# Optimization experiments

Measured on AMD Instinct MI355X. Metric: run time of the kernel, lower is better.

The kernel has to match this reference:

```python
import jax, jax.numpy as jnp
import numpy as np

K_SIZE = 7
D_MODEL = 128
D_Q = 64
N_HEADS = 4
D_FF = 512
EPS = 1e-5


def _windows(x, k):
    # x: [N,E,H,W] -> [N,E,P,H,W]; zero-padded local k x k windows,
    # row-major over (dy,dx), matching nn.Unfold ordering.
    p = k // 2
    N, E, H, W = x.shape
    xp = jnp.pad(x, ((0, 0), (0, 0), (p, p), (p, p)))
    ws = [xp[:, :, i:i + H, j:j + W] for i in range(k) for j in range(k)]
    return jnp.stack(ws, axis=2)


def _layernorm(x, g, b):
    m = jnp.mean(x, -1, keepdims=True)
    v = jnp.var(x, -1, keepdims=True)
    return (x - m) * jax.lax.rsqrt(v + EPS) * g + b


def setup_inputs() -> dict:
    key = jax.random.key(0)
    ks = jax.random.split(key, 12)
    E, Q, F = D_MODEL, D_Q, D_FF

    def g(k, shape, s=0.02):
        return jax.random.normal(k, shape, jnp.float32) * s

    return dict(
        x=jax.random.normal(ks[0], (4, E, 64, 64), jnp.float32),
        qcoeff=jax.random.normal(ks[1], (4, Q), jnp.float32),
        wq=g(ks[2], (E, E)), bq=jnp.zeros((E,), jnp.float32),
        wk=g(ks[3], (E, E)), bk=jnp.zeros((E,), jnp.float32),
        wv=g(ks[4], (E, E)), bv=jnp.zeros((E,), jnp.float32),
        rel_bias=jnp.zeros((N_HEADS, K_SIZE * K_SIZE), jnp.float32),
        ln1_g=jnp.ones((E,), jnp.float32), ln1_b=jnp.zeros((E,), jnp.float32),
        bil_w=g(ks[5], (E, E, Q)), bil_b=jnp.zeros((E,), jnp.float32),
        ln2_g=jnp.ones((E,), jnp.float32), ln2_b=jnp.zeros((E,), jnp.float32),
        w1=g(ks[6], (F, E)), b1=jnp.zeros((F,), jnp.float32),
        w2=g(ks[7], (E, F)), b2=jnp.zeros((E,), jnp.float32),
    )


def reference(x, qcoeff, wq, bq, wk, bk, wv, bv, rel_bias, ln1_g, ln1_b,
              bil_w, bil_b, ln2_g, ln2_b, w1, b1, w2, b2):
    N, E, H, W = x.shape
    Nh = N_HEADS
    Hd = E // Nh
    P = K_SIZE * K_SIZE

    x_nhwc = jnp.transpose(x, (0, 2, 3, 1))              # [N,H,W,E]
    xn = _layernorm(x_nhwc, ln1_g, ln1_b)
    xnc = jnp.transpose(xn, (0, 3, 1, 2))                # [N,E,H,W]

    # 1x1-conv projections
    q = jnp.einsum('nchw,oc->nohw', xnc, wq) + bq[None, :, None, None]
    k = jnp.einsum('nchw,oc->nohw', xnc, wk) + bk[None, :, None, None]
    v = jnp.einsum('nchw,oc->nohw', xnc, wv) + bv[None, :, None, None]

    # local windows of K/V: [N,Nh,Hd,P,H,W]
    Kw = _windows(k, K_SIZE).reshape(N, Nh, Hd, P, H, W)
    Vw = _windows(v, K_SIZE).reshape(N, Nh, Hd, P, H, W)
    Qh = q.reshape(N, Nh, Hd, H, W)

    scores = jnp.einsum('nhdyx,nhdpyx->nhpyx', Qh, Kw)
    scores = scores + rel_bias[None, :, :, None, None]
    attn = jax.nn.softmax(scores, axis=2)                # softmax over P
    out = jnp.einsum('nhpyx,nhdpyx->nhdyx', attn, Vw).reshape(N, E, H, W)
    z0 = jnp.transpose(out, (0, 2, 3, 1))                # [N,H,W,E]

    # Bilinear(z0, qcoeff): qcoeff constant per (H,W) -> contract once per batch
    t = jnp.einsum('oiq,nq->noi', bil_w, qcoeff)         # [N,E,E]
    z1 = jnp.einsum('nhwi,noi->nhwo', z0, t) + bil_b

    z2 = z1 + x_nhwc
    z3 = _layernorm(z2, ln2_g, ln2_b)
    h1 = jax.nn.gelu(z3 @ w1.T + b1, approximate=False)  # dropout inactive (eval)
    z4 = h1 @ w2.T + b2 + z2
    return jnp.transpose(z4, (0, 3, 1, 2))               # [N,E,H,W]
```

## Files before the change

### kernel.cpp

```cpp
#include <hip/hip_runtime.h>
#include <cmath>

#define EPS 1e-5f
#define SZ 2097152

typedef __attribute__((ext_vector_type(8))) short short8;
typedef __attribute__((ext_vector_type(4))) float floatx4;

__device__ __forceinline__ float dot4(float4 a, float4 b) {
  return fmaf(a.x, b.x, fmaf(a.y, b.y, fmaf(a.z, b.z, a.w * b.w)));
}

__device__ __forceinline__ short f2bf(float f) {
  union { float f; unsigned u; } v; v.f = f;
  unsigned r = v.u + 0x7fff + ((v.u >> 16) & 1);
  return (short)(r >> 16);
}

#define MFMA16(a, b, c) __builtin_amdgcn_mfma_f32_16x16x32_bf16(a, b, c, 0, 0, 0)

__global__ __launch_bounds__(256) void k_prep(const float* __restrict__ w1,
    const float* __restrict__ w2, const float* __restrict__ wq,
    const float* __restrict__ wk, const float* __restrict__ wv,
    const float* __restrict__ bil_w, const float* __restrict__ qcoeff,
    short* __restrict__ w1bf, short* __restrict__ w2bf,
    short* __restrict__ wqbf, short* __restrict__ wkbf, short* __restrict__ wvbf,
    short* __restrict__ tb) {
  __shared__ float qs[256];
  int tid = threadIdx.x;
  qs[tid] = qcoeff[tid];
  __syncthreads();
  int tid0 = blockIdx.x * 256 + tid;
  int stride = gridDim.x * 256;
  for (int i = tid0; i < 16384; i += stride) {
    int flat = i * 4; int f = flat >> 7, c = flat & 127;
    float4 v = *(const float4*)&w1[flat];
    short t4[4] = {f2bf(v.x), f2bf(v.y), f2bf(v.z), f2bf(v.w)};
    *(uint2*)&w1bf[f * 136 + c] = *(uint2*)t4;
  }
  for (int i = tid0; i < 16384; i += stride) {
    int flat = i * 4; int o = flat >> 9, j = flat & 511;
    int ck = j >> 7, jj = j & 127;
    float4 v = *(const float4*)&w2[flat];
    short t4[4] = {f2bf(v.x), f2bf(v.y), f2bf(v.z), f2bf(v.w)};
    *(uint2*)&w2bf[(ck * 128 + o) * 136 + jj] = *(uint2*)t4;
  }
  for (int i = tid0; i < 4096; i += stride) {
    int flat = i * 4; int o = flat >> 7, c = flat & 127;
    float4 a = *(const float4*)&wq[flat];
    float4 b = *(const float4*)&wk[flat];
    float4 cc = *(const float4*)&wv[flat];
    short ta[4] = {f2bf(a.x), f2bf(a.y), f2bf(a.z), f2bf(a.w)};
    short tb4[4] = {f2bf(b.x), f2bf(b.y), f2bf(b.z), f2bf(b.w)};
    short tc[4] = {f2bf(cc.x), f2bf(cc.y), f2bf(cc.z), f2bf(cc.w)};
    *(uint2*)&wqbf[o * 136 + c] = *(uint2*)ta;
    *(uint2*)&wkbf[o * 136 + c] = *(uint2*)tb4;
    *(uint2*)&wvbf[o * 136 + c] = *(uint2*)tc;
  }
  for (int flat = tid0; flat < 16384; flat += stride) {
    const float* wrow = bil_w + (size_t)flat * 64;
    float acc[4] = {0.f, 0.f, 0.f, 0.f};
    for (int qq = 0; qq < 64; qq += 4) {
      float4 w4 = *(const float4*)&wrow[qq];
#pragma unroll
      for (int nn = 0; nn < 4; ++nn) {
        const float* qc = &qs[nn * 64 + qq];
        acc[nn] = fmaf(w4.x, qc[0], fmaf(w4.y, qc[1], fmaf(w4.z, qc[2], fmaf(w4.w, qc[3], acc[nn]))));
      }
    }
    int o = flat >> 7, i = flat & 127;
#pragma unroll
    for (int nn = 0; nn < 4; ++nn) tb[nn * 17408 + o * 136 + i] = f2bf(acc[nn]);
  }
}

__global__ __launch_bounds__(512) void k_qkvln(const float* __restrict__ x,
    const float* __restrict__ g, const float* __restrict__ b,
    const short* __restrict__ wqbf, const short* __restrict__ wkbf,
    const short* __restrict__ wvbf, const float* __restrict__ bq,
    const float* __restrict__ bk, const float* __restrict__ bv,
    float* __restrict__ xnhwc, short* __restrict__ qbf,
    short* __restrict__ kbf, short* __restrict__ vtb) {
  __shared__ float tile[128 * 33];
  __shared__ float mres[32], rres[32];
  __shared__ __align__(16) short xs[32 * 136];
  __shared__ __align__(16) short ws[128 * 136];
  int tid = threadIdx.x;
  int bid = blockIdx.x;
  int half = bid & 1, ny = bid >> 1;
  int n = ny >> 6, y = ny & 63;
  const float* xb = x + (size_t)n * 524288 + y * 64 + half * 32;
  for (int it = 0; it < 8; ++it) {
    int flat = it * 512 + tid;
    int c = flat >> 5, xpl = flat & 31;
    tile[c * 33 + xpl] = xb[(size_t)c * 4096 + xpl];
  }
  __syncthreads();
  {
    int pxl = tid >> 4, cl = tid & 15;
    float s = 0.f, sq = 0.f;
#pragma unroll
    for (int j = 0; j < 8; ++j) {
      float v = tile[(cl * 8 + j) * 33 + pxl];
      s += v; sq += v * v;
    }
    s += __shfl_xor(s, 1);  sq += __shfl_xor(sq, 1);
    s += __shfl_xor(s, 2);  sq += __shfl_xor(sq, 2);
    s += __shfl_xor(s, 4);  sq += __shfl_xor(sq, 4);
    s += __shfl_xor(s, 8);  sq += __shfl_xor(sq, 8);
    if (cl == 0) {
      float m = s * (1.f / 128.f);
      float var = sq * (1.f / 128.f) - m * m;
      mres[pxl] = m;
      rres[pxl] = rsqrtf(var + EPS);
    }
  }
  __syncthreads();
  size_t rowbase = (size_t)ny * 8192 + half * 4096;
  for (int it = 0; it < 8; ++it) {
    int flat = it * 512 + tid;
    int c = flat & 127, pxl = flat >> 7;
    float v = tile[c * 33 + pxl];
    xnhwc[rowbase + flat] = v;
    xs[pxl * 136 + c] = f2bf((v - mres[pxl]) * rres[pxl] * g[c] + b[c]);
  }
  __syncthreads();
  int w = tid >> 6, lane = tid & 63;
  int quad = lane >> 4, r16 = lane & 15;
  int wm = w & 1, wn = w >> 1;
  int stripl = wm * 16;
  short8 a[4];
#pragma unroll
  for (int kk = 0; kk < 4; ++kk)
    a[kk] = *(const short8*)&xs[(stripl + r16) * 136 + kk * 32 + quad * 8];
  const short* wptr[3] = {wqbf, wkbf, wvbf};
  const float* bptr[3] = {bq, bk, bv};
  for (int m = 0; m < 3; ++m) {
    __syncthreads();
    const short* wp = wptr[m];
    for (int i = tid; i < 2176; i += 512)
      *(short8*)&ws[i * 8] = *(const short8*)&wp[i * 8];
    __syncthreads();
    const float* bb = bptr[m];
#pragma unroll
    for (int nt = 0; nt < 2; ++nt) {
      int o0 = wn * 32 + nt * 16;
      floatx4 acc = {0.f, 0.f, 0.f, 0.f};
#pragma unroll
      for (int kk = 0; kk < 4; ++kk) {
        short8 bfr = *(const short8*)&ws[(o0 + r16) * 136 + kk * 32 + quad * 8];
        acc = MFMA16(a[kk], bfr, acc);
      }
      float bv2 = bb[o0 + r16];
      if (m < 2) {
        short* dst = (m == 0) ? qbf : kbf;
#pragma unroll
        for (int r = 0; r < 4; ++r) {
          int pxl = stripl + quad * 4 + r;
          dst[rowbase + pxl * 128 + o0 + r16] = f2bf(acc[r] + bv2);
        }
      } else {
        short t4[4] = {f2bf(acc[0] + bv2), f2bf(acc[1] + bv2),
                       f2bf(acc[2] + bv2), f2bf(acc[3] + bv2)};
        *(uint2*)&vtb[(size_t)(n * 128 + o0 + r16) * 4096 + y * 64 + half * 32 +
                      stripl + quad * 4] = *(uint2*)t4;
      }
    }
  }
}

__global__ __launch_bounds__(512, 4) void k_at(const short* __restrict__ qbf,
    const short* __restrict__ kbf, const short* __restrict__ vtb,
    const float* __restrict__ rel_bias, const short* __restrict__ tb,
    const float* __restrict__ bil_b, const float* __restrict__ xnhwc,
    const float* __restrict__ g2, const float* __restrict__ b2ln,
    const short* __restrict__ w1bf, const float* __restrict__ b1,
    const short* __restrict__ w2bf, const float* __restrict__ b2,
    float* __restrict__ out) {
  __shared__ __align__(16) char smem[70272];
  short* h1s = (short*)smem;
  short* z3s = (short*)(smem + 44672);
  float* z2s = (float*)(smem + 53376);
  int tid = threadIdx.x;
  int bid = blockIdx.x;
  int half = bid & 1, ny = bid >> 1;
  int n = ny >> 6, y = ny & 63;
  int w16 = tid >> 6, lane = tid & 63;
  int quad = lane >> 4, r16 = lane & 15;
  size_t rowbase = (size_t)ny * 8192;
  int wm = w16 & 1, wn = w16 >> 1;
  int stripL = wm * 16;
  const short* tn = tb + (size_t)n * 17408;
  float xres[2][4];
#pragma unroll
  for (int nt = 0; nt < 2; ++nt)
#pragma unroll
    for (int r = 0; r < 4; ++r)
      xres[nt][r] = xnhwc[rowbase + (half * 32 + stripL + quad * 4 + r) * 128 +
                          wn * 32 + nt * 16 + r16];
  short8 tf[2][4];
  {
    int h = w16 >> 1, swl = w16 & 1;
    int sg = half * 2 + swl;
    int strip = sg * 16;
    float* ssfw = (float*)(smem + w16 * 3200);
    short* Abw = (short*)(smem + 25600 + w16 * 2176);
    float* biasw = (float*)(smem + 43008 + w16 * 208);
    const short* qrow = qbf + (size_t)n * 524288 + (size_t)y * 8192 + h * 32;
    const short* kbp = kbf + (size_t)n * 524288 + h * 32;
    short8 qf = *(const short8*)&qrow[(strip + r16) * 128 + quad * 8];
    short8 kf[7][2];
#pragma unroll
    for (int r = 0; r < 7; ++r) {
      int yyc = min(max(y + r - 3, 0), 63);
#pragma unroll
      for (int t = 0; t < 2; ++t) {
        int gxc = min(max((sg + t) * 16 + r16 - 3, 0), 63);
        kf[r][t] = *(const short8*)&kbp[(size_t)(yyc * 64 + gxc) * 128 + quad * 8];
      }
    }
    {
      unsigned* ad = (unsigned*)Abw;
      for (int i = lane; i < 544; i += 64) ad[i] = 0u;
    }
    if (lane < 49) biasw[lane] = rel_bias[h * 49 + lane];
#pragma unroll
    for (int r = 0; r < 7; ++r) {
      bool yok = (unsigned)(y + r - 3) < 64u;
#pragma unroll
      for (int t = 0; t < 2; ++t) {
        int xxc = (sg + t) * 16 + r16;
        bool ok = yok && ((unsigned)(xxc - 3) < 64u);
        floatx4 c = MFMA16(qf, kf[r][t], ((floatx4){0.f, 0.f, 0.f, 0.f}));
#pragma unroll
        for (int rr = 0; rr < 4; ++rr) {
          int lrow = quad * 4 + rr;
          int dx = xxc - (strip + lrow);
          if ((unsigned)dx < 7u) {
            float val = ok ? c[rr] : 0.f;
            ssfw[lrow * 50 + r * 7 + dx] = val + biasw[r * 7 + dx];
          }
        }
      }
    }
    {
      int lrow = lane >> 2, sub = lane & 3;
      int p0 = sub * 12;
      float sv[13];
      float mx = -1e30f;
#pragma unroll
      for (int pi = 0; pi < 13; ++pi) {
        sv[pi] = ssfw[lrow * 50 + p0 + pi];
        mx = fmaxf(mx, sv[pi]);
      }
      mx = fmaxf(mx, __shfl_xor(mx, 1));
      mx = fmaxf(mx, __shfl_xor(mx, 2));
      float sum = 0.f;
#pragma unroll
      for (int pi = 0; pi < 13; ++pi) {
        float e = __expf(sv[pi] - mx);
        if (pi == 12 && sub != 3) e = 0.f;
        sv[pi] = e; sum += e;
      }
      sum += __shfl_xor(sum, 1);
      sum += __shfl_xor(sum, 2);
      float inv = 1.f / sum;
#pragma unroll
      for (int pi = 0; pi < 13; ++pi)
        if (pi < 12 || sub == 3) ssfw[lrow * 50 + p0 + pi] = sv[pi] * inv;
    }
    floatx4 oacc[2] = {(floatx4){0.f, 0.f, 0.f, 0.f}, (floatx4){0.f, 0.f, 0.f, 0.f}};
    int lrow = lane >> 2, sub = lane & 3;
    int pxg = strip + lrow;
    const short* vbp = vtb + (size_t)(n * 128 + h * 32) * 4096;
    short8 vf[2][2][2];
    {
      int yyc0 = min(max(y - 3, 0), 63);
#pragma unroll
      for (int kk = 0; kk < 2; ++kk)
#pragma unroll
        for (int nt = 0; nt < 2; ++nt)
          vf[0][kk][nt] = *(const short8*)&vbp[(size_t)(nt * 16 + r16) * 4096 + yyc0 * 64 + kk * 32 + quad * 8];
    }
#pragma unroll
    for (int r = 0; r < 7; ++r) {
      if (r < 6) {
        int yycn = min(max(y + r - 2, 0), 63);
#pragma unroll
        for (int kk = 0; kk < 2; ++kk)
#pragma unroll
          for (int nt = 0; nt < 2; ++nt)
            vf[(r + 1) & 1][kk][nt] = *(const short8*)&vbp[(size_t)(nt * 16 + r16) * 4096 + yycn * 64 + kk * 32 + quad * 8];
      }
      int c0 = pxg + sub - 3;
      if ((unsigned)c0 < 64u) Abw[lrow * 68 + c0] = f2bf(ssfw[lrow * 50 + r * 7 + sub]);
      int c1 = pxg + sub + 1;
      if (sub < 3 && (unsigned)c1 < 64u)
        Abw[lrow * 68 + c1] = f2bf(ssfw[lrow * 50 + r * 7 + sub + 4]);
      if ((unsigned)(y + r - 3) < 64u) {
#pragma unroll
        for (int kk = 0; kk < 2; ++kk) {
          short8 af = *(const short8*)&Abw[r16 * 68 + kk * 32 + quad * 8];
#pragma unroll
          for (int nt = 0; nt < 2; ++nt)
            oacc[nt] = MFMA16(af, vf[r & 1][kk][nt], oacc[nt]);
        }
      }
    }
#pragma unroll
    for (int nt = 0; nt < 2; ++nt)
#pragma unroll
      for (int kk = 0; kk < 4; ++kk)
        tf[nt][kk] = *(const short8*)&tn[(wn * 32 + nt * 16 + r16) * 136 + kk * 32 + quad * 8];
#pragma unroll
    for (int nt = 0; nt < 2; ++nt)
#pragma unroll
      for (int rr = 0; rr < 4; ++rr) {
        int pxl = swl * 16 + quad * 4 + rr;
        z3s[pxl * 136 + h * 32 + nt * 16 + r16] = f2bf(oacc[nt][rr]);
      }
  }
  __syncthreads();
  {
    short8 a[4];
#pragma unroll
    for (int kk = 0; kk < 4; ++kk)
      a[kk] = *(const short8*)&z3s[(stripL + r16) * 136 + kk * 32 + quad * 8];
#pragma unroll
    for (int nt = 0; nt < 2; ++nt) {
      int o0 = wn * 32 + nt * 16;
      floatx4 acc = {0.f, 0.f, 0.f, 0.f};
#pragma unroll
      for (int kk = 0; kk < 4; ++kk)
        acc = MFMA16(a[kk], tf[nt][kk], acc);
      float bb = bil_b[o0 + r16];
#pragma unroll
      for (int r = 0; r < 4; ++r) {
        int pxl = stripL + quad * 4 + r;
        z2s[pxl * 132 + o0 + r16] = acc[r] + bb + xres[nt][r];
      }
    }
  }
  __syncthreads();
  short8 wA[2][4];
#pragma unroll
  for (int nt = 0; nt < 2; ++nt)
#pragma unroll
    for (int kk = 0; kk < 4; ++kk)
      wA[nt][kk] = *(const short8*)&w1bf[(wn * 32 + nt * 16 + r16) * 136 + kk * 32 + quad * 8];
  {
    int px = tid >> 4, cl = tid & 15;
    float4 v0 = *(const float4*)&z2s[px * 132 + cl * 8];
    float4 v1 = *(const float4*)&z2s[px * 132 + cl * 8 + 4];
    float s = v0.x + v0.y + v0.z + v0.w + v1.x + v1.y + v1.z + v1.w;
    float sq = dot4(v0, v0) + dot4(v1, v1);
    s += __shfl_xor(s, 1);  sq += __shfl_xor(sq, 1);
    s += __shfl_xor(s, 2);  sq += __shfl_xor(sq, 2);
    s += __shfl_xor(s, 4);  sq += __shfl_xor(sq, 4);
    s += __shfl_xor(s, 8);  sq += __shfl_xor(sq, 8);
    float m = s * (1.f / 128.f);
    float var = sq * (1.f / 128.f) - m * m;
    float rr = rsqrtf(var + EPS);
    int c0 = cl * 8;
    short t8[8];
#pragma unroll
    for (int j = 0; j < 8; ++j) {
      float vv = (j < 4) ? (&v0.x)[j] : (&v1.x)[j - 4];
      t8[j] = f2bf((vv - m) * rr * g2[c0 + j] + b2ln[c0 + j]);
    }
    *(uint4*)&z3s[px * 136 + c0] = *(uint4*)t8;
  }
  __syncthreads();
  floatx4 zacc[2];
  zacc[0] = (floatx4){0.f, 0.f, 0.f, 0.f};
  zacc[1] = (floatx4){0.f, 0.f, 0.f, 0.f};
  for (int fc = 0; fc < 512; fc += 128) {
    short8 wB[2][4];
#pragma unroll
    for (int nt = 0; nt < 2; ++nt)
#pragma unroll
      for (int kk = 0; kk < 4; ++kk)
        wB[nt][kk] = *(const short8*)&w2bf[((fc >> 7) * 128 + wn * 32 + nt * 16 + r16) * 136 + kk * 32 + quad * 8];
    float bb1v[2];
    bb1v[0] = b1[fc + wn * 32 + r16];
    bb1v[1] = b1[fc + wn * 32 + 16 + r16];
    short8 a3[4];
#pragma unroll
    for (int kk = 0; kk < 4; ++kk)
      a3[kk] = *(const short8*)&z3s[(stripL + r16) * 136 + kk * 32 + quad * 8];
    floatx4 hacc[2];
#pragma unroll
    for (int nt = 0; nt < 2; ++nt) {
      hacc[nt] = (floatx4){0.f, 0.f, 0.f, 0.f};
#pragma unroll
      for (int kk = 0; kk < 4; ++kk)
        hacc[nt] = MFMA16(a3[kk], wA[nt][kk], hacc[nt]);
    }
    if (fc < 384) {
#pragma unroll
      for (int nt = 0; nt < 2; ++nt)
#pragma unroll
        for (int kk = 0; kk < 4; ++kk)
          wA[nt][kk] = *(const short8*)&w1bf[(fc + 128 + wn * 32 + nt * 16 + r16) * 136 + kk * 32 + quad * 8];
    }
#pragma unroll
    for (int nt = 0; nt < 2; ++nt) {
      int f0 = wn * 32 + nt * 16;
#pragma unroll
      for (int r = 0; r < 4; ++r) {
        float hv = hacc[nt][r] + bb1v[nt];
        float ge = 0.5f * hv * (1.f + erff(hv * 0.70710678118f));
        h1s[(stripL + quad * 4 + r) * 136 + f0 + r16] = f2bf(ge);
      }
    }
    __syncthreads();
    short8 ah[4];
#pragma unroll
    for (int kk = 0; kk < 4; ++kk)
      ah[kk] = *(const short8*)&h1s[(stripL + r16) * 136 + kk * 32 + quad * 8];
#pragma unroll
    for (int nt = 0; nt < 2; ++nt)
#pragma unroll
      for (int kk = 0; kk < 4; ++kk)
        zacc[nt] = MFMA16(ah[kk], wB[nt][kk], zacc[nt]);
    __syncthreads();
  }
#pragma unroll
  for (int nt = 0; nt < 2; ++nt) {
    int o = wn * 32 + nt * 16 + r16;
    float bb = b2[o];
    float res[4];
#pragma unroll
    for (int r = 0; r < 4; ++r)
      res[r] = zacc[nt][r] + bb + z2s[(stripL + quad * 4 + r) * 132 + o];
    *(float4*)&out[(((size_t)(n * 128 + o)) * 64 + y) * 64 + half * 32 + stripL + quad * 4] =
        *(float4*)res;
  }
}

extern "C" void kernel_launch(void* const* d_in, const int* in_sizes, int n_in,
                              void* d_out, int out_size, void* d_ws, size_t ws_size,
                              hipStream_t stream) {
  const float* x        = (const float*)d_in[0];
  const float* qcoeff   = (const float*)d_in[1];
  const float* wq       = (const float*)d_in[2];
  const float* bq       = (const float*)d_in[3];
  const float* wk       = (const float*)d_in[4];
  const float* bk       = (const float*)d_in[5];
  const float* wv       = (const float*)d_in[6];
  const float* bv       = (const float*)d_in[7];
  const float* rel_bias = (const float*)d_in[8];
  const float* ln1_g    = (const float*)d_in[9];
  const float* ln1_b    = (const float*)d_in[10];
  const float* bil_w    = (const float*)d_in[11];
  const float* bil_b    = (const float*)d_in[12];
  const float* ln2_g    = (const float*)d_in[13];
  const float* ln2_b    = (const float*)d_in[14];
  const float* w1       = (const float*)d_in[15];
  const float* b1       = (const float*)d_in[16];
  const float* w2       = (const float*)d_in[17];
  const float* b2       = (const float*)d_in[18];
  float* out = (float*)d_out;

  float* ws = (float*)d_ws;
  float* x_nhwc = ws;
  short* qbf = (short*)(ws + 2 * SZ);
  short* kbf = qbf + SZ;
  short* vtb = kbf + SZ;
  short* bf     = (short*)(ws + 4 * SZ);
  short* tb     = bf;
  short* w1bf   = bf + 4 * 17408;
  short* w2bf   = w1bf + 512 * 136;
  short* wqbf   = w2bf + 4 * 17408;
  short* wkbf   = wqbf + 17408;
  short* wvbf   = wkbf + 17408;

  k_prep<<<256, 256, 0, stream>>>(w1, w2, wq, wk, wv, bil_w, qcoeff,
                                  w1bf, w2bf, wqbf, wkbf, wvbf, tb);
  k_qkvln<<<512, 512, 0, stream>>>(x, ln1_g, ln1_b, wqbf, wkbf, wvbf,
                                   bq, bk, bv, x_nhwc, qbf, kbf, vtb);
  k_at<<<512, 512, 0, stream>>>(qbf, kbf, vtb, rel_bias, tb, bil_b, x_nhwc,
                                ln2_g, ln2_b, w1bf, b1, w2bf, b2, out);
}
```

Measured before the change: 151.0 us.

## Split fused attention/MLP kernel into separate attention and tail kernels with XCD banding

Splits the fused local-attention plus bilinear/LN/MLP kernel into two kernels: k_attn writes the attention output z3 to a global bf16 buffer, and k_tail reads it back for the bilinear, layernorm and FFN stages. Each kernel uses less shared memory and fewer registers, which allows different occupancy targets (launch bounds 3 and 8). It also remaps block indices so that consecutive image rows land on the same XCD, improving L2 reuse of neighbouring K/V rows. The cost is an extra kernel launch and a global round trip for the z3 intermediate.

After: 188.2 us. 1.25x slower.

```diff
diff --git a/kernel.cpp b/kernel.cpp
--- a/kernel.cpp
+++ b/kernel.cpp
@@ -15,6 +15,10 @@
   union { float f; unsigned u; } v; v.f = f;
   unsigned r = v.u + 0x7fff + ((v.u >> 16) & 1);
   return (short)(r >> 16);
+}
+
+__device__ __forceinline__ int xcd_band(int bid) {
+  return (bid & 7) * 64 + (bid >> 3);
 }
 
 #define MFMA16(a, b, c) __builtin_amdgcn_mfma_f32_16x16x32_bf16(a, b, c, 0, 0, 0)
@@ -86,8 +90,8 @@
   __shared__ __align__(16) short xs[32 * 136];
   __shared__ __align__(16) short ws[128 * 136];
   int tid = threadIdx.x;
-  int bid = blockIdx.x;
-  int half = bid & 1, ny = bid >> 1;
+  int l = xcd_band(blockIdx.x);
+  int half = l & 1, ny = l >> 1;
   int n = ny >> 6, y = ny & 63;
   const float* xb = x + (size_t)n * 524288 + y * 64 + half * 32;
   for (int it = 0; it < 8; ++it) {
@@ -169,21 +173,146 @@
   }
 }
 
-__global__ __launch_bounds__(512, 4) void k_at(const short* __restrict__ qbf,
+__global__ __launch_bounds__(512, 3) void k_attn(const short* __restrict__ qbf,
     const short* __restrict__ kbf, const short* __restrict__ vtb,
-    const float* __restrict__ rel_bias, const short* __restrict__ tb,
-    const float* __restrict__ bil_b, const float* __restrict__ xnhwc,
-    const float* __restrict__ g2, const float* __restrict__ b2ln,
-    const short* __restrict__ w1bf, const float* __restrict__ b1,
-    const short* __restrict__ w2bf, const float* __restrict__ b2,
-    float* __restrict__ out) {
-  __shared__ __align__(16) char smem[70272];
-  short* h1s = (short*)smem;
-  short* z3s = (short*)(smem + 44672);
-  float* z2s = (float*)(smem + 53376);
+    const float* __restrict__ rel_bias, short* __restrict__ z3g) {
+  __shared__ __align__(16) char smem[44672];
   int tid = threadIdx.x;
-  int bid = blockIdx.x;
-  int half = bid & 1, ny = bid >> 1;
+  int l = xcd_band(blockIdx.x);
+  int half = l & 1, ny = l >> 1;
+  int n = ny >> 6, y = ny & 63;
+  int w16 = tid >> 6, lane = tid & 63;
+  int quad = lane >> 4, r16 = lane & 15;
+  size_t rowbase = (size_t)ny * 8192;
+  int h = w16 >> 1, swl = w16 & 1;
+  int sg = half * 2 + swl;
+  int strip = sg * 16;
+  float* ssfw = (float*)(smem + w16 * 3200);
+  short* Abw = (short*)(smem + 25600 + w16 * 2176);
+  float* biasw = (float*)(smem + 43008 + w16 * 208);
+  const short* qrow = qbf + (size_t)n * 524288 + (size_t)y * 8192 + h * 32;
+  const short* kbp = kbf + (size_t)n * 524288 + h * 32;
+  short8 qf = *(const short8*)&qrow[(strip + r16) * 128 + quad * 8];
+  short8 kf[7][2];
+#pragma unroll
+  for (int r = 0; r < 7; ++r) {
+    int yyc = min(max(y + r - 3, 0), 63);
+#pragma unroll
+    for (int t = 0; t < 2; ++t) {
+      int gxc = min(max((sg + t) * 16 + r16 - 3, 0), 63);
+      kf[r][t] = *(const short8*)&kbp[(size_t)(yyc * 64 + gxc) * 128 + quad * 8];
+    }
+  }
+  {
+    unsigned* ad = (unsigned*)Abw;
+    for (int i = lane; i < 544; i += 64) ad[i] = 0u;
+  }
+  if (lane < 49) biasw[lane] = rel_bias[h * 49 + lane];
+#pragma unroll
+  for (int r = 0; r < 7; ++r) {
+    bool yok = (unsigned)(y + r - 3) < 64u;
+#pragma unroll
+    for (int t = 0; t < 2; ++t) {
+      int xxc = (sg + t) * 16 + r16;
+      bool ok = yok && ((unsigned)(xxc - 3) < 64u);
+      floatx4 c = MFMA16(qf, kf[r][t], ((floatx4){0.f, 0.f, 0.f, 0.f}));
+#pragma unroll
+      for (int rr = 0; rr < 4; ++rr) {
+        int lrow = quad * 4 + rr;
+        int dx = xxc - (strip + lrow);
+        if ((unsigned)dx < 7u) {
+          float val = ok ? c[rr] : 0.f;
+          ssfw[lrow * 50 + r * 7 + dx] = val + biasw[r * 7 + dx];
+        }
+      }
+    }
+  }
+  {
+    int lrow = lane >> 2, sub = lane & 3;
+    int p0 = sub * 12;
+    float sv[13];
+    float mx = -1e30f;
+#pragma unroll
+    for (int pi = 0; pi < 13; ++pi) {
+      sv[pi] = ssfw[lrow * 50 + p0 + pi];
+      mx = fmaxf(mx, sv[pi]);
+    }
+    mx = fmaxf(mx, __shfl_xor(mx, 1));
+    mx = fmaxf(mx, __shfl_xor(mx, 2));
+    float sum = 0.f;
+#pragma unroll
+    for (int pi = 0; pi < 13; ++pi) {
+      float e = __expf(sv[pi] - mx);
+      if (pi == 12 && sub != 3) e = 0.f;
+      sv[pi] = e; sum += e;
+    }
+    sum += __shfl_xor(sum, 1);
+    sum += __shfl_xor(sum, 2);
+    float inv = 1.f / sum;
+#pragma unroll
+    for (int pi = 0; pi < 13; ++pi)
+      if (pi < 12 || sub == 3) ssfw[lrow * 50 + p0 + pi] = sv[pi] * inv;
+  }
+  floatx4 oacc[2] = {(floatx4){0.f, 0.f, 0.f, 0.f}, (floatx4){0.f, 0.f, 0.f, 0.f}};
+  int lrow = lane >> 2, sub = lane & 3;
+  int pxg = strip + lrow;
+  const short* vbp = vtb + (size_t)(n * 128 + h * 32) * 4096;
+  short8 vf[2][2][2];
+  {
+    int yyc0 = min(max(y - 3, 0), 63);
+#pragma unroll
+    for (int kk = 0; kk < 2; ++kk)
+#pragma unroll
+      for (int nt = 0; nt < 2; ++nt)
+        vf[0][kk][nt] = *(const short8*)&vbp[(size_t)(nt * 16 + r16) * 4096 + yyc0 * 64 + kk * 32 + quad * 8];
+  }
+#pragma unroll
+  for (int r = 0; r < 7; ++r) {
+    if (r < 6) {
+      int yycn = min(max(y + r - 2, 0), 63);
+#pragma unroll
+      for (int kk = 0; kk < 2; ++kk)
+#pragma unroll
+        for (int nt = 0; nt < 2; ++nt)
+          vf[(r + 1) & 1][kk][nt] = *(const short8*)&vbp[(size_t)(nt * 16 + r16) * 4096 + yycn * 64 + kk * 32 + quad * 8];
+    }
+    int c0 = pxg + sub - 3;
+    if ((unsigned)c0 < 64u) Abw[lrow * 68 + c0] = f2bf(ssfw[lrow * 50 + r * 7 + sub]);
+    int c1 = pxg + sub + 1;
+    if (sub < 3 && (unsigned)c1 < 64u)
+      Abw[lrow * 68 + c1] = f2bf(ssfw[lrow * 50 + r * 7 + sub + 4]);
+    if ((unsigned)(y + r - 3) < 64u) {
+#pragma unroll
+      for (int kk = 0; kk < 2; ++kk) {
+        short8 af = *(const short8*)&Abw[r16 * 68 + kk * 32 + quad * 8];
+#pragma unroll
+        for (int nt = 0; nt < 2; ++nt)
+          oacc[nt] = MFMA16(af, vf[r & 1][kk][nt], oacc[nt]);
+      }
+    }
+  }
+#pragma unroll
+  for (int nt = 0; nt < 2; ++nt)
+#pragma unroll
+    for (int rr = 0; rr < 4; ++rr) {
+      int px = half * 32 + swl * 16 + quad * 4 + rr;
+      z3g[rowbase + px * 128 + h * 32 + nt * 16 + r16] = f2bf(oacc[nt][rr]);
+    }
+}
+
+__global__ __launch_bounds__(512, 8) void k_tail(const short* __restrict__ z3g,
+    const short* __restrict__ tb, const float* __restrict__ bil_b,
+    const float* __restrict__ xnhwc, const float* __restrict__ g2,
+    const float* __restrict__ b2ln, const short* __restrict__ w1bf,
+    const float* __restrict__ b1, const short* __restrict__ w2bf,
+    const float* __restrict__ b2, float* __restrict__ out) {
+  __shared__ __align__(16) char smem[34304];
+  short* z3s = (short*)smem;
+  float* z2s = (float*)(smem + 8704);
+  short* h1s = (short*)(smem + 25600);
+  int tid = threadIdx.x;
+  int l = xcd_band(blockIdx.x);
+  int half = l & 1, ny = l >> 1;
   int n = ny >> 6, y = ny & 63;
   int w16 = tid >> 6, lane = tid & 63;
   int quad = lane >> 4, r16 = lane & 15;
@@ -191,6 +320,12 @@
   int wm = w16 & 1, wn = w16 >> 1;
   int stripL = wm * 16;
   const short* tn = tb + (size_t)n * 17408;
+  short8 tf[2][4];
+#pragma unroll
+  for (int nt = 0; nt < 2; ++nt)
+#pragma unroll
+    for (int kk = 0; kk < 4; ++kk)
+      tf[nt][kk] = *(const short8*)&tn[(wn * 32 + nt * 16 + r16) * 136 + kk * 32 + quad * 8];
   float xres[2][4];
 #pragma unroll
   for (int nt = 0; nt < 2; ++nt)
@@ -198,134 +333,11 @@
     for (int r = 0; r < 4; ++r)
       xres[nt][r] = xnhwc[rowbase + (half * 32 + stripL + quad * 4 + r) * 128 +
                           wn * 32 + nt * 16 + r16];
-  short8 tf[2][4];
-  {
-    int h = w16 >> 1, swl = w16 & 1;
-    int sg = half * 2 + swl;
-    int strip = sg * 16;
-    float* ssfw = (float*)(smem + w16 * 3200);
-    short* Abw = (short*)(smem + 25600 + w16 * 2176);
-    float* biasw = (float*)(smem + 43008 + w16 * 208);
-    const short* qrow = qbf + (size_t)n * 524288 + (size_t)y * 8192 + h * 32;
-    const short* kbp = kbf + (size_t)n * 524288 + h * 32;
-    short8 qf = *(const short8*)&qrow[(strip + r16) * 128 + quad * 8];
-    short8 kf[7][2];
-#pragma unroll
-    for (int r = 0; r < 7; ++r) {
-      int yyc = min(max(y + r - 3, 0), 63);
-#pragma unroll
-      for (int t = 0; t < 2; ++t) {
-        int gxc = min(max((sg + t) * 16 + r16 - 3, 0), 63);
-        kf[r][t] = *(const short8*)&kbp[(size_t)(yyc * 64 + gxc) * 128 + quad * 8];
-      }
-    }
-    {
-      unsigned* ad = (unsigned*)Abw;
-      for (int i = lane; i < 544; i += 64) ad[i] = 0u;
-    }
-    if (lane < 49) biasw[lane] = rel_bias[h * 49 + lane];
-#pragma unroll
-    for (int r = 0; r < 7; ++r) {
-      bool yok = (unsigned)(y + r - 3) < 64u;
-#pragma unroll
-      for (int t = 0; t < 2; ++t) {
-        int xxc = (sg + t) * 16 + r16;
-        bool ok = yok && ((unsigned)(xxc - 3) < 64u);
-        floatx4 c = MFMA16(qf, kf[r][t], ((floatx4){0.f, 0.f, 0.f, 0.f}));
-#pragma unroll
-        for (int rr = 0; rr < 4; ++rr) {
-          int lrow = quad * 4 + rr;
-          int dx = xxc - (strip + lrow);
-          if ((unsigned)dx < 7u) {
-            float val = ok ? c[rr] : 0.f;
-            ssfw[lrow * 50 + r * 7 + dx] = val + biasw[r * 7 + dx];
-          }
-        }
-      }
-    }
-    {
-      int lrow = lane >> 2, sub = lane & 3;
-      int p0 = sub * 12;
-      float sv[13];
-      float mx = -1e30f;
-#pragma unroll
-      for (int pi = 0; pi < 13; ++pi) {
-        sv[pi] = ssfw[lrow * 50 + p0 + pi];
-        mx = fmaxf(mx, sv[pi]);
-      }
-      mx = fmaxf(mx, __shfl_xor(mx, 1));
-      mx = fmaxf(mx, __shfl_xor(mx, 2));
-      float sum = 0.f;
-#pragma unroll
-      for (int pi = 0; pi < 13; ++pi) {
-        float e = __expf(sv[pi] - mx);
-        if (pi == 12 && sub != 3) e = 0.f;
-        sv[pi] = e; sum += e;
-      }
-      sum += __shfl_xor(sum, 1);
-      sum += __shfl_xor(sum, 2);
-      float inv = 1.f / sum;
-#pragma unroll
-      for (int pi = 0; pi < 13; ++pi)
-        if (pi < 12 || sub == 3) ssfw[lrow * 50 + p0 + pi] = sv[pi] * inv;
-    }
-    floatx4 oacc[2] = {(floatx4){0.f, 0.f, 0.f, 0.f}, (floatx4){0.f, 0.f, 0.f, 0.f}};
-    int lrow = lane >> 2, sub = lane & 3;
-    int pxg = strip + lrow;
-    const short* vbp = vtb + (size_t)(n * 128 + h * 32) * 4096;
-    short8 vf[2][2][2];
-    {
-      int yyc0 = min(max(y - 3, 0), 63);
-#pragma unroll
-      for (int kk = 0; kk < 2; ++kk)
-#pragma unroll
-        for (int nt = 0; nt < 2; ++nt)
-          vf[0][kk][nt] = *(const short8*)&vbp[(size_t)(nt * 16 + r16) * 4096 + yyc0 * 64 + kk * 32 + quad * 8];
-    }
-#pragma unroll
-    for (int r = 0; r < 7; ++r) {
-      if (r < 6) {
-        int yycn = min(max(y + r - 2, 0), 63);
-#pragma unroll
-        for (int kk = 0; kk < 2; ++kk)
-#pragma unroll
-          for (int nt = 0; nt < 2; ++nt)
-            vf[(r + 1) & 1][kk][nt] = *(const short8*)&vbp[(size_t)(nt * 16 + r16) * 4096 + yycn * 64 + kk * 32 + quad * 8];
-      }
-      int c0 = pxg + sub - 3;
-      if ((unsigned)c0 < 64u) Abw[lrow * 68 + c0] = f2bf(ssfw[lrow * 50 + r * 7 + sub]);
-      int c1 = pxg + sub + 1;
-      if (sub < 3 && (unsigned)c1 < 64u)
-        Abw[lrow * 68 + c1] = f2bf(ssfw[lrow * 50 + r * 7 + sub + 4]);
-      if ((unsigned)(y + r - 3) < 64u) {
-#pragma unroll
-        for (int kk = 0; kk < 2; ++kk) {
-          short8 af = *(const short8*)&Abw[r16 * 68 + kk * 32 + quad * 8];
-#pragma unroll
-          for (int nt = 0; nt < 2; ++nt)
-            oacc[nt] = MFMA16(af, vf[r & 1][kk][nt], oacc[nt]);
-        }
-      }
-    }
-#pragma unroll
-    for (int nt = 0; nt < 2; ++nt)
-#pragma unroll
-      for (int kk = 0; kk < 4; ++kk)
-        tf[nt][kk] = *(const short8*)&tn[(wn * 32 + nt * 16 + r16) * 136 + kk * 32 + quad * 8];
-#pragma unroll
-    for (int nt = 0; nt < 2; ++nt)
-#pragma unroll
-      for (int rr = 0; rr < 4; ++rr) {
-        int pxl = swl * 16 + quad * 4 + rr;
-        z3s[pxl * 136 + h * 32 + nt * 16 + r16] = f2bf(oacc[nt][rr]);
-      }
-  }
-  __syncthreads();
   {
     short8 a[4];
 #pragma unroll
     for (int kk = 0; kk < 4; ++kk)
-      a[kk] = *(const short8*)&z3s[(stripL + r16) * 136 + kk * 32 + quad * 8];
+      a[kk] = *(const short8*)&z3g[rowbase + (half * 32 + stripL + r16) * 128 + kk * 32 + quad * 8];
 #pragma unroll
     for (int nt = 0; nt < 2; ++nt) {
       int o0 = wn * 32 + nt * 16;
@@ -474,11 +486,13 @@
   short* wqbf   = w2bf + 4 * 17408;
   short* wkbf   = wqbf + 17408;
   short* wvbf   = wkbf + 17408;
+  short* z3g    = wvbf + 17408;
 
   k_prep<<<256, 256, 0, stream>>>(w1, w2, wq, wk, wv, bil_w, qcoeff,
                                   w1bf, w2bf, wqbf, wkbf, wvbf, tb);
   k_qkvln<<<512, 512, 0, stream>>>(x, ln1_g, ln1_b, wqbf, wkbf, wvbf,
                                    bq, bk, bv, x_nhwc, qbf, kbf, vtb);
-  k_at<<<512, 512, 0, stream>>>(qbf, kbf, vtb, rel_bias, tb, bil_b, x_nhwc,
-                                ln2_g, ln2_b, w1bf, b1, w2bf, b2, out);
-}
+  k_attn<<<512, 512, 0, stream>>>(qbf, kbf, vtb, rel_bias, z3g);
+  k_tail<<<512, 512, 0, stream>>>(z3g, tb, bil_b, x_nhwc, ln2_g, ln2_b,
+                                  w1bf, b1, w2bf, b2, out);
+}
```

## Fold weight prep into QKV kernel and remap blocks across XCDs

Applied to the files above, without the earlier changes.

Removes the separate k_prep launch. The QKV+LayerNorm kernel now converts wq/wk/wv to bf16 straight into shared memory, and its threads also convert w1/w2 and contract the bilinear weights with qcoeff as trailing work. This removes one kernel launch and its serialization. Both kernels also remap block IDs so that consecutive rows land on the same XCD, which is meant to improve L2 locality. The cost is that each of the 512 blocks redundantly converts the QKV weights from fp32, and the bilinear contraction now reads qcoeff from global memory per thread.

Result: slower. 155.3 us (+2.9%).

```diff
diff --git a/kernel.cpp b/kernel.cpp
--- a/kernel.cpp
+++ b/kernel.cpp
@@ -17,77 +17,29 @@
   return (short)(r >> 16);
 }
 
+__device__ __forceinline__ int xcd_band(int bid) {
+  return (bid & 7) * 64 + (bid >> 3);
+}
+
 #define MFMA16(a, b, c) __builtin_amdgcn_mfma_f32_16x16x32_bf16(a, b, c, 0, 0, 0)
-
-__global__ __launch_bounds__(256) void k_prep(const float* __restrict__ w1,
-    const float* __restrict__ w2, const float* __restrict__ wq,
-    const float* __restrict__ wk, const float* __restrict__ wv,
-    const float* __restrict__ bil_w, const float* __restrict__ qcoeff,
-    short* __restrict__ w1bf, short* __restrict__ w2bf,
-    short* __restrict__ wqbf, short* __restrict__ wkbf, short* __restrict__ wvbf,
-    short* __restrict__ tb) {
-  __shared__ float qs[256];
-  int tid = threadIdx.x;
-  qs[tid] = qcoeff[tid];
-  __syncthreads();
-  int tid0 = blockIdx.x * 256 + tid;
-  int stride = gridDim.x * 256;
-  for (int i = tid0; i < 16384; i += stride) {
-    int flat = i * 4; int f = flat >> 7, c = flat & 127;
-    float4 v = *(const float4*)&w1[flat];
-    short t4[4] = {f2bf(v.x), f2bf(v.y), f2bf(v.z), f2bf(v.w)};
-    *(uint2*)&w1bf[f * 136 + c] = *(uint2*)t4;
-  }
-  for (int i = tid0; i < 16384; i += stride) {
-    int flat = i * 4; int o = flat >> 9, j = flat & 511;
-    int ck = j >> 7, jj = j & 127;
-    float4 v = *(const float4*)&w2[flat];
-    short t4[4] = {f2bf(v.x), f2bf(v.y), f2bf(v.z), f2bf(v.w)};
-    *(uint2*)&w2bf[(ck * 128 + o) * 136 + jj] = *(uint2*)t4;
-  }
-  for (int i = tid0; i < 4096; i += stride) {
-    int flat = i * 4; int o = flat >> 7, c = flat & 127;
-    float4 a = *(const float4*)&wq[flat];
-    float4 b = *(const float4*)&wk[flat];
-    float4 cc = *(const float4*)&wv[flat];
-    short ta[4] = {f2bf(a.x), f2bf(a.y), f2bf(a.z), f2bf(a.w)};
-    short tb4[4] = {f2bf(b.x), f2bf(b.y), f2bf(b.z), f2bf(b.w)};
-    short tc[4] = {f2bf(cc.x), f2bf(cc.y), f2bf(cc.z), f2bf(cc.w)};
-    *(uint2*)&wqbf[o * 136 + c] = *(uint2*)ta;
-    *(uint2*)&wkbf[o * 136 + c] = *(uint2*)tb4;
-    *(uint2*)&wvbf[o * 136 + c] = *(uint2*)tc;
-  }
-  for (int flat = tid0; flat < 16384; flat += stride) {
-    const float* wrow = bil_w + (size_t)flat * 64;
-    float acc[4] = {0.f, 0.f, 0.f, 0.f};
-    for (int qq = 0; qq < 64; qq += 4) {
-      float4 w4 = *(const float4*)&wrow[qq];
-#pragma unroll
-      for (int nn = 0; nn < 4; ++nn) {
-        const float* qc = &qs[nn * 64 + qq];
-        acc[nn] = fmaf(w4.x, qc[0], fmaf(w4.y, qc[1], fmaf(w4.z, qc[2], fmaf(w4.w, qc[3], acc[nn]))));
-      }
-    }
-    int o = flat >> 7, i = flat & 127;
-#pragma unroll
-    for (int nn = 0; nn < 4; ++nn) tb[nn * 17408 + o * 136 + i] = f2bf(acc[nn]);
-  }
-}
 
 __global__ __launch_bounds__(512) void k_qkvln(const float* __restrict__ x,
     const float* __restrict__ g, const float* __restrict__ b,
-    const short* __restrict__ wqbf, const short* __restrict__ wkbf,
-    const short* __restrict__ wvbf, const float* __restrict__ bq,
+    const float* __restrict__ wq, const float* __restrict__ wk,
+    const float* __restrict__ wv, const float* __restrict__ bq,
     const float* __restrict__ bk, const float* __restrict__ bv,
+    const float* __restrict__ w1, const float* __restrict__ w2,
+    const float* __restrict__ bil_w, const float* __restrict__ qcoeff,
     float* __restrict__ xnhwc, short* __restrict__ qbf,
-    short* __restrict__ kbf, short* __restrict__ vtb) {
+    short* __restrict__ kbf, short* __restrict__ vtb,
+    short* __restrict__ w1bf, short* __restrict__ w2bf, short* __restrict__ tb) {
   __shared__ float tile[128 * 33];
   __shared__ float mres[32], rres[32];
   __shared__ __align__(16) short xs[32 * 136];
   __shared__ __align__(16) short ws[128 * 136];
   int tid = threadIdx.x;
-  int bid = blockIdx.x;
-  int half = bid & 1, ny = bid >> 1;
+  int l = xcd_band(blockIdx.x);
+  int half = l & 1, ny = l >> 1;
   int n = ny >> 6, y = ny & 63;
   const float* xb = x + (size_t)n * 524288 + y * 64 + half * 32;
   for (int it = 0; it < 8; ++it) {
@@ -133,13 +85,20 @@
 #pragma unroll
   for (int kk = 0; kk < 4; ++kk)
     a[kk] = *(const short8*)&xs[(stripl + r16) * 136 + kk * 32 + quad * 8];
-  const short* wptr[3] = {wqbf, wkbf, wvbf};
+  const float* wptr[3] = {wq, wk, wv};
   const float* bptr[3] = {bq, bk, bv};
   for (int m = 0; m < 3; ++m) {
     __syncthreads();
-    const short* wp = wptr[m];
-    for (int i = tid; i < 2176; i += 512)
-      *(short8*)&ws[i * 8] = *(const short8*)&wp[i * 8];
+    const float* wp = wptr[m];
+    for (int i = tid; i < 2048; i += 512) {
+      int e = i * 8;
+      float4 v0 = *(const float4*)&wp[e];
+      float4 v1 = *(const float4*)&wp[e + 4];
+      short t8[8] = {f2bf(v0.x), f2bf(v0.y), f2bf(v0.z), f2bf(v0.w),
+                     f2bf(v1.x), f2bf(v1.y), f2bf(v1.z), f2bf(v1.w)};
+      int o = e >> 7, c = e & 127;
+      *(uint4*)&ws[o * 136 + c] = *(uint4*)t8;
+    }
     __syncthreads();
     const float* bb = bptr[m];
 #pragma unroll
@@ -166,6 +125,34 @@
                       stripl + quad * 4] = *(uint2*)t4;
       }
     }
+  }
+  int gtid = blockIdx.x * 512 + tid;
+  if (gtid < 8192) {
+    int e = gtid * 8, f = e >> 7, c = e & 127;
+    float4 v0 = *(const float4*)&w1[e], v1 = *(const float4*)&w1[e + 4];
+    short t8[8] = {f2bf(v0.x), f2bf(v0.y), f2bf(v0.z), f2bf(v0.w),
+                   f2bf(v1.x), f2bf(v1.y), f2bf(v1.z), f2bf(v1.w)};
+    *(uint4*)&w1bf[f * 136 + c] = *(uint4*)t8;
+  } else if (gtid < 16384) {
+    int e = (gtid - 8192) * 8, o = e >> 9, j = e & 511, ck = j >> 7, jj = j & 127;
+    float4 v0 = *(const float4*)&w2[e], v1 = *(const float4*)&w2[e + 4];
+    short t8[8] = {f2bf(v0.x), f2bf(v0.y), f2bf(v0.z), f2bf(v0.w),
+                   f2bf(v1.x), f2bf(v1.y), f2bf(v1.z), f2bf(v1.w)};
+    *(uint4*)&w2bf[(ck * 128 + o) * 136 + jj] = *(uint4*)t8;
+  } else if (gtid < 81920) {
+    int idx = gtid - 16384;
+    int nn = idx >> 14, oi = idx & 16383;
+    const float* wrow = bil_w + (size_t)oi * 64;
+    const float* qc = qcoeff + nn * 64;
+    float acc = 0.f;
+#pragma unroll
+    for (int q = 0; q < 64; q += 4) {
+      float4 w4 = *(const float4*)&wrow[q];
+      float4 q4 = *(const float4*)&qc[q];
+      acc = fmaf(w4.x, q4.x, fmaf(w4.y, q4.y, fmaf(w4.z, q4.z, fmaf(w4.w, q4.w, acc))));
+    }
+    int o = oi >> 7, i = oi & 127;
+    tb[nn * 17408 + o * 136 + i] = f2bf(acc);
   }
 }
 
@@ -182,8 +169,8 @@
   short* z3s = (short*)(smem + 44672);
   float* z2s = (float*)(smem + 53376);
   int tid = threadIdx.x;
-  int bid = blockIdx.x;
-  int half = bid & 1, ny = bid >> 1;
+  int l = xcd_band(blockIdx.x);
+  int half = l & 1, ny = l >> 1;
   int n = ny >> 6, y = ny & 63;
   int w16 = tid >> 6, lane = tid & 63;
   int quad = lane >> 4, r16 = lane & 15;
@@ -471,14 +458,10 @@
   short* tb     = bf;
   short* w1bf   = bf + 4 * 17408;
   short* w2bf   = w1bf + 512 * 136;
-  short* wqbf   = w2bf + 4 * 17408;
-  short* wkbf   = wqbf + 17408;
-  short* wvbf   = wkbf + 17408;
-
-  k_prep<<<256, 256, 0, stream>>>(w1, w2, wq, wk, wv, bil_w, qcoeff,
-                                  w1bf, w2bf, wqbf, wkbf, wvbf, tb);
-  k_qkvln<<<512, 512, 0, stream>>>(x, ln1_g, ln1_b, wqbf, wkbf, wvbf,
-                                   bq, bk, bv, x_nhwc, qbf, kbf, vtb);
+
+  k_qkvln<<<512, 512, 0, stream>>>(x, ln1_g, ln1_b, wq, wk, wv, bq, bk, bv,
+                                   w1, w2, bil_w, qcoeff,
+                                   x_nhwc, qbf, kbf, vtb, w1bf, w2bf, tb);
   k_at<<<512, 512, 0, stream>>>(qbf, kbf, vtb, rel_bias, tb, bil_b, x_nhwc,
                                 ln2_g, ln2_b, w1bf, b1, w2bf, b2, out);
 }
```
